# Kernel optimization log

Measured on AMD Instinct MI355X. Metric: run time of the kernel, lower is better.

The kernel has to match this reference:

```python
import jax, jax.numpy as jnp
import numpy as np

# Mamba2 hyperparams derived from init_kwargs
D_MODEL = 512
FF = 2048
D_STATE = 128
D_CONV = 4
EXPAND = 2
D_INNER = EXPAND * D_MODEL          # 1024
HEADDIM = 64                        # mamba_ssm Mamba2 default
NHEADS = D_INNER // HEADDIM         # 16
NGROUPS = 1                         # default
CONV_DIM = D_INNER + 2 * NGROUPS * D_STATE      # 1280
D_IN_PROJ = 2 * D_INNER + 2 * NGROUPS * D_STATE + NHEADS  # 2320
B_SZ = 2
SEQ = 2048


def setup_inputs() -> dict:
    key = jax.random.key(0)
    ks = jax.random.split(key, 10)
    s = 0.02
    return dict(
        tgt=jax.random.normal(ks[0], (B_SZ, SEQ, D_MODEL), jnp.float32),
        W_in=jax.random.normal(ks[1], (D_MODEL, D_IN_PROJ), jnp.float32) * s,
        conv_w=jax.random.normal(ks[2], (CONV_DIM, D_CONV), jnp.float32) * s,
        conv_b=jnp.zeros((CONV_DIM,), jnp.float32),
        dt_bias=jax.random.uniform(ks[3], (NHEADS,), jnp.float32, -4.0, -1.0),
        A_log=jnp.log(jax.random.uniform(ks[4], (NHEADS,), jnp.float32, 1.0, 16.0)),
        D_skip=jnp.ones((NHEADS,), jnp.float32),
        gnorm_w=jnp.ones((D_INNER,), jnp.float32),
        W_out=jax.random.normal(ks[5], (D_INNER, D_MODEL), jnp.float32) * s,
        n1_g=jnp.ones((D_MODEL,), jnp.float32), n1_b=jnp.zeros((D_MODEL,), jnp.float32),
        ffn_w1=jax.random.normal(ks[6], (D_MODEL, FF), jnp.float32) * s,
        ffn_b1=jnp.zeros((FF,), jnp.float32),
        ffn_w2=jax.random.normal(ks[7], (FF, D_MODEL), jnp.float32) * s,
        ffn_b2=jnp.zeros((D_MODEL,), jnp.float32),
        n3_g=jnp.ones((D_MODEL,), jnp.float32), n3_b=jnp.zeros((D_MODEL,), jnp.float32),
    )


def _layernorm(x, g, b, eps=1e-5):
    m = jnp.mean(x, -1, keepdims=True)
    v = jnp.var(x, -1, keepdims=True)
    return (x - m) * jax.lax.rsqrt(v + eps) * g + b


def _mamba2(x, W_in, conv_w, conv_b, dt_bias, A_log, D_skip, gnorm_w, W_out):
    Bb, S, _ = x.shape
    zxbcdt = x @ W_in                               # (B,S,2320)
    z = zxbcdt[..., :D_INNER]                       # gate (B,S,1024)
    xBC = zxbcdt[..., D_INNER:D_INNER + CONV_DIM]   # (B,S,1280)
    dt = zxbcdt[..., D_INNER + CONV_DIM:]           # (B,S,H)
    # causal depthwise conv1d (kernel D_CONV) + SiLU
    xc = jnp.moveaxis(xBC, 1, 2)                    # (B,C,S)
    xp = jnp.pad(xc, ((0, 0), (0, 0), (D_CONV - 1, 0)))
    yc = sum(conv_w[None, :, k:k + 1] * xp[:, :, k:k + S] for k in range(D_CONV))
    xBC = jax.nn.silu(jnp.moveaxis(yc, 1, 2) + conv_b)
    xs = xBC[..., :D_INNER].reshape(Bb, S, NHEADS, HEADDIM)   # (B,S,H,P)
    Bc = xBC[..., D_INNER:D_INNER + D_STATE]                  # (B,S,N)
    Cc = xBC[..., D_INNER + D_STATE:]                         # (B,S,N)
    dt = jax.nn.softplus(dt + dt_bias)                        # (B,S,H)
    A = -jnp.exp(A_log)                                       # (H,)
    dA = jnp.exp(dt * A)                                      # (B,S,H)
    tm = lambda a: jnp.moveaxis(a, 1, 0)                      # time-major

    def step(h, inp):
        # h: (B,H,P,N) selective state
        dA_t, dt_t, B_t, C_t, x_t = inp
        h = h * dA_t[:, :, None, None] \
            + (dt_t[:, :, None] * x_t)[..., None] * B_t[:, None, None, :]
        y_t = jnp.einsum('bhpn,bn->bhp', h, C_t)
        return h, y_t

    h0 = jnp.zeros((Bb, NHEADS, HEADDIM, D_STATE), x.dtype)
    _, ys = jax.lax.scan(step, h0, (tm(dA), tm(dt), tm(Bc), tm(Cc), tm(xs)))
    y = jnp.moveaxis(ys, 0, 1) + D_skip[None, None, :, None] * xs
    y = y.reshape(Bb, S, D_INNER)
    # gated RMSNorm (norm_before_gate=False): norm(y * silu(z)) * w
    y = y * jax.nn.silu(z)
    y = y * jax.lax.rsqrt(jnp.mean(y * y, -1, keepdims=True) + 1e-5) * gnorm_w
    return y @ W_out


def reference(tgt, W_in, conv_w, conv_b, dt_bias, A_log, D_skip, gnorm_w, W_out,
              n1_g, n1_b, ffn_w1, ffn_b1, ffn_w2, ffn_b2, n3_g, n3_b):
    t = tgt + _mamba2(tgt, W_in, conv_w, conv_b, dt_bias, A_log, D_skip, gnorm_w, W_out)
    t = _layernorm(t, n1_g, n1_b)
    h = jax.nn.gelu(t @ ffn_w1 + ffn_b1, approximate=False) @ ffn_w2 + ffn_b2
    return _layernorm(t + h, n3_g, n3_b)
```

## Files before the change

kernel.cpp:

```cpp
#include <hip/hip_runtime.h>
#include <hip/hip_bf16.h>
#include <cstddef>
#include <cstdint>

#define D_MODEL   512
#define FF        2048
#define D_STATE   128
#define D_INNER   1024
#define HEADDIM   64
#define NHEADS    16
#define CONV_DIM  1280
#define D_IN_PROJ 2320
#define NPJ_PAD   2432
#define B_SZ      2
#define SEQ       2048
#define NTOK      (B_SZ*SEQ)
#define LCH       32
#define NCHUNK    (SEQ/LCH)
#define NCID      (B_SZ*NHEADS*NCHUNK)

typedef __attribute__((ext_vector_type(8))) short short8;
typedef __attribute__((ext_vector_type(4))) float f32x4;

__device__ __forceinline__ float sigmoid_f(float x){ return 1.0f/(1.0f+expf(-x)); }
__device__ __forceinline__ float gelu_f(float x){ return 0.5f*x*(1.0f+erff(x*0.70710678118654752f)); }

__device__ __forceinline__ unsigned short bf16bits(float f){
  __hip_bfloat16 h = __float2bfloat16(f);
  return *reinterpret_cast<unsigned short*>(&h);
}
__device__ __forceinline__ float bf2f(unsigned short u){ return __uint_as_float(((unsigned)u)<<16); }
__device__ __forceinline__ float blo(unsigned u){ return __uint_as_float(u<<16); }
__device__ __forceinline__ float bhi(unsigned u){ return __uint_as_float(u & 0xffff0000u); }
__device__ __forceinline__ unsigned bfpack2(float a, float b){
  return (unsigned)bf16bits(a) | ((unsigned)bf16bits(b)<<16);
}

__device__ __forceinline__ void gload16(const void* g, void* l){
  __builtin_amdgcn_global_load_lds((const __attribute__((address_space(1))) void*)g,
                                   (__attribute__((address_space(3))) void*)l, 16, 0, 0);
}

union U4S8 { uint4 v; unsigned short s[8]; };

template<int EPI, typename OT>
__global__ __launch_bounds__(256)
void gemm128(const __hip_bfloat16* __restrict__ A, const __hip_bfloat16* __restrict__ Bt,
             const float* __restrict__ bias, OT* __restrict__ C,
             int N, int K, int ldc)
{
  __shared__ char AsRaw[128*128];
  __shared__ char BsRaw[128*128];

  const int t    = threadIdx.x;
  const int bm   = blockIdx.y * 128;
  const int bn   = blockIdx.x * 128;
  const int lane = t & 63;
  const int wid  = t >> 6;
  const int wr   = wid >> 1;
  const int wc   = wid & 1;
  const int lrow = lane & 15;
  const int lkb  = (lane >> 4) * 16;
  const int sw   = (lrow & 7) << 4;

  const int rA  = t >> 3;
  const int cbA = (t & 7) * 16;
  const int scb = cbA ^ ((rA & 7) << 4);
  const size_t strideA = (size_t)K * 2;
  const char* aSrc = (const char*)A  + (size_t)(bm + rA) * strideA + scb;
  const char* bSrc = (const char*)Bt + (size_t)(bn + rA) * strideA + scb;
  char* aDst = AsRaw + wid * 1024;
  char* bDst = BsRaw + wid * 1024;

  f32x4 acc[4][4];
  #pragma unroll
  for (int m=0;m<4;m++)
    #pragma unroll
    for (int n=0;n<4;n++) acc[m][n] = (f32x4){0.f,0.f,0.f,0.f};

  const char* ArP = AsRaw + (wr*64 + lrow) * 128;
  const char* BrP = BsRaw + (wc*64 + lrow) * 128;

  for (int k0 = 0; k0 < K; k0 += 64) {
    const size_t ko = (size_t)k0 * 2;
    gload16(aSrc + ko,               aDst);
    gload16(aSrc + ko + 32*strideA,  aDst + 4096);
    gload16(aSrc + ko + 64*strideA,  aDst + 8192);
    gload16(aSrc + ko + 96*strideA,  aDst + 12288);
    gload16(bSrc + ko,               bDst);
    gload16(bSrc + ko + 32*strideA,  bDst + 4096);
    gload16(bSrc + ko + 64*strideA,  bDst + 8192);
    gload16(bSrc + ko + 96*strideA,  bDst + 12288);
    __syncthreads();
    #pragma unroll
    for (int kk = 0; kk < 2; ++kk) {
      const int kb = (kk*64 + lkb) ^ sw;
      short8 a0 = *(const short8*)(ArP + 0*2048 + kb);
      short8 a1 = *(const short8*)(ArP + 1*2048 + kb);
      short8 a2 = *(const short8*)(ArP + 2*2048 + kb);
      short8 a3 = *(const short8*)(ArP + 3*2048 + kb);
      short8 b0 = *(const short8*)(BrP + 0*2048 + kb);
      short8 b1 = *(const short8*)(BrP + 1*2048 + kb);
      short8 b2 = *(const short8*)(BrP + 2*2048 + kb);
      short8 b3 = *(const short8*)(BrP + 3*2048 + kb);
      #pragma unroll
      for (int m=0;m<4;m++){
        short8 am = (m==0)?a0:(m==1)?a1:(m==2)?a2:a3;
        acc[m][0] = __builtin_amdgcn_mfma_f32_16x16x32_bf16(am, b0, acc[m][0], 0,0,0);
        acc[m][1] = __builtin_amdgcn_mfma_f32_16x16x32_bf16(am, b1, acc[m][1], 0,0,0);
        acc[m][2] = __builtin_amdgcn_mfma_f32_16x16x32_bf16(am, b2, acc[m][2], 0,0,0);
        acc[m][3] = __builtin_amdgcn_mfma_f32_16x16x32_bf16(am, b3, acc[m][3], 0,0,0);
      }
    }
    __syncthreads();
  }

  const int orow0 = bm + wr*64 + (lane >> 4) * 4;
  const int ocol0 = bn + wc*64 + lrow;
  #pragma unroll
  for (int n=0;n<4;n++) {
    const int col = ocol0 + n*16;
    if (col >= N) continue;
    const float bv = (EPI>=1) ? bias[col] : 0.f;
    #pragma unroll
    for (int m=0;m<4;m++) {
      #pragma unroll
      for (int j=0;j<4;j++) {
        float v = acc[m][n][j] + bv;
        if (EPI==2) v = gelu_f(v);
        OT* cp = C + (size_t)(orow0 + m*16 + j)*ldc + col;
        if constexpr (sizeof(OT)==2) *cp = __float2bfloat16(v); else *cp = v;
      }
    }
  }
}

template<int EPI, typename OT>
__global__ __launch_bounds__(256)
void gemm_bf16(const __hip_bfloat16* __restrict__ A, const __hip_bfloat16* __restrict__ Bt,
               const float* __restrict__ bias, OT* __restrict__ C,
               int N, int K, int ldc)
{
  __shared__ char AsRaw[128*128];
  __shared__ char BsRaw[64*128];

  const int t    = threadIdx.x;
  const int bm   = blockIdx.y * 128;
  const int bn   = blockIdx.x * 64;
  const int lane = t & 63;
  const int wid  = t >> 6;
  const int wr   = wid >> 1;
  const int wc   = wid & 1;
  const int lrow = lane & 15;
  const int lkb  = (lane >> 4) * 16;
  const int sw   = (lrow & 7) << 4;

  const int rA  = t >> 3;
  const int cbA = (t & 7) * 16;
  const int scb = cbA ^ ((rA & 7) << 4);
  const size_t strideA = (size_t)K * 2;
  const char* aSrc = (const char*)A  + (size_t)(bm + rA) * strideA + scb;
  const char* bSrc = (const char*)Bt + (size_t)(bn + rA) * strideA + scb;
  char* aDst = AsRaw + wid * 1024;
  char* bDst = BsRaw + wid * 1024;

  f32x4 acc[4][2];
  #pragma unroll
  for (int m=0;m<4;m++)
    #pragma unroll
    for (int n=0;n<2;n++) acc[m][n] = (f32x4){0.f,0.f,0.f,0.f};

  const char* ArP = AsRaw + (wr*64 + lrow) * 128;
  const char* BrP = BsRaw + (wc*32 + lrow) * 128;

  for (int k0 = 0; k0 < K; k0 += 64) {
    const size_t ko = (size_t)k0 * 2;
    gload16(aSrc + ko,               aDst);
    gload16(aSrc + ko + 32*strideA,  aDst + 4096);
    gload16(aSrc + ko + 64*strideA,  aDst + 8192);
    gload16(aSrc + ko + 96*strideA,  aDst + 12288);
    gload16(bSrc + ko,               bDst);
    gload16(bSrc + ko + 32*strideA,  bDst + 4096);
    __syncthreads();
    #pragma unroll
    for (int kk = 0; kk < 2; ++kk) {
      const int kb = (kk*64 + lkb) ^ sw;
      short8 a0 = *(const short8*)(ArP + 0*2048 + kb);
      short8 a1 = *(const short8*)(ArP + 1*2048 + kb);
      short8 a2 = *(const short8*)(ArP + 2*2048 + kb);
      short8 a3 = *(const short8*)(ArP + 3*2048 + kb);
      short8 b0 = *(const short8*)(BrP + 0*2048 + kb);
      short8 b1 = *(const short8*)(BrP + 1*2048 + kb);
      acc[0][0] = __builtin_amdgcn_mfma_f32_16x16x32_bf16(a0, b0, acc[0][0], 0,0,0);
      acc[1][0] = __builtin_amdgcn_mfma_f32_16x16x32_bf16(a1, b0, acc[1][0], 0,0,0);
      acc[2][0] = __builtin_amdgcn_mfma_f32_16x16x32_bf16(a2, b0, acc[2][0], 0,0,0);
      acc[3][0] = __builtin_amdgcn_mfma_f32_16x16x32_bf16(a3, b0, acc[3][0], 0,0,0);
      acc[0][1] = __builtin_amdgcn_mfma_f32_16x16x32_bf16(a0, b1, acc[0][1], 0,0,0);
      acc[1][1] = __builtin_amdgcn_mfma_f32_16x16x32_bf16(a1, b1, acc[1][1], 0,0,0);
      acc[2][1] = __builtin_amdgcn_mfma_f32_16x16x32_bf16(a2, b1, acc[2][1], 0,0,0);
      acc[3][1] = __builtin_amdgcn_mfma_f32_16x16x32_bf16(a3, b1, acc[3][1], 0,0,0);
    }
    __syncthreads();
  }

  const int orow0 = bm + wr*64 + (lane >> 4) * 4;
  const int ocol0 = bn + wc*32 + lrow;
  #pragma unroll
  for (int n=0;n<2;n++) {
    const int col = ocol0 + n*16;
    if (col >= N) continue;
    const float bv = (EPI>=1) ? bias[col] : 0.f;
    #pragma unroll
    for (int m=0;m<4;m++) {
      #pragma unroll
      for (int j=0;j<4;j++) {
        float v = acc[m][n][j] + bv;
        if (EPI==2) v = gelu_f(v);
        OT* cp = C + (size_t)(orow0 + m*16 + j)*ldc + col;
        if constexpr (sizeof(OT)==2) *cp = __float2bfloat16(v); else *cp = v;
      }
    }
  }
}

__global__ __launch_bounds__(256)
void transpose_to_bf16(const float* __restrict__ in, __hip_bfloat16* __restrict__ out,
                       int K, int N, int Npad)
{
  __shared__ float tbuf[32][33];
  const int bx = blockIdx.x * 32;
  const int by = blockIdx.y * 32;
  const int tx = threadIdx.x & 31, ty = threadIdx.x >> 5;
  #pragma unroll
  for (int u=0;u<4;u++){
    int k = by + ty + u*8;
    int n = bx + tx;
    tbuf[ty+u*8][tx] = (n < N) ? in[(size_t)k*N + n] : 0.f;
  }
  __syncthreads();
  #pragma unroll
  for (int u=0;u<4;u++){
    int n = bx + ty + u*8;
    int k = by + tx;
    if (n < Npad) out[(size_t)n*K + k] = __float2bfloat16(tbuf[tx][ty+u*8]);
  }
}

__global__ __launch_bounds__(256)
void f32_to_bf16_k(const float* __restrict__ in, __hip_bfloat16* __restrict__ out, int n)
{
  int i = (blockIdx.x*256 + threadIdx.x)*4;
  if (i < n) {
    float4 v = *(const float4*)(in + i);
    out[i+0]=__float2bfloat16(v.x); out[i+1]=__float2bfloat16(v.y);
    out[i+2]=__float2bfloat16(v.z); out[i+3]=__float2bfloat16(v.w);
  }
}

__global__ __launch_bounds__(256)
void conv_silu(const float* __restrict__ zx, const float* __restrict__ cw,
               const float* __restrict__ cb, __hip_bfloat16* __restrict__ xbc,
               const float* __restrict__ dt_bias, float* __restrict__ dtp)
{
  const int c  = blockIdx.x*256 + threadIdx.x;
  const int t0 = blockIdx.y*64;
  const int b  = blockIdx.z;
  const float w0=cw[c*4+0], w1=cw[c*4+1], w2=cw[c*4+2], w3=cw[c*4+3];
  const float cbv = cb[c];
  const float* base = zx + ((size_t)(b*SEQ + t0))*D_IN_PROJ + D_INNER + c;
  __hip_bfloat16* obase = xbc + ((size_t)(b*SEQ + t0))*CONV_DIM + c;
  float xm3, xm2, xm1;
  if (t0 == 0) { xm3 = 0.f; xm2 = 0.f; xm1 = 0.f; }
  else {
    xm3 = base[-3*(ptrdiff_t)D_IN_PROJ];
    xm2 = base[-2*(ptrdiff_t)D_IN_PROJ];
    xm1 = base[-1*(ptrdiff_t)D_IN_PROJ];
  }
  #pragma unroll 4
  for (int t=0; t<64; ++t) {
    float xc = base[(size_t)t*D_IN_PROJ];
    float acc = cbv + w0*xm3 + w1*xm2 + w2*xm1 + w3*xc;
    obase[(size_t)t*CONV_DIM] = __float2bfloat16(acc * sigmoid_f(acc));
    xm3 = xm2; xm2 = xm1; xm1 = xc;
  }
  if (blockIdx.x == 0) {
    #pragma unroll
    for (int it=0; it<4; ++it) {
      int idx = it*256 + threadIdx.x;
      int tloc = idx >> 4, hh = idx & 15;
      int tok = b*SEQ + t0 + tloc;
      float x = zx[(size_t)tok*D_IN_PROJ + (D_INNER + CONV_DIM) + hh] + dt_bias[hh];
      float sp = (x > 20.f) ? x : log1pf(expf(x));
      dtp[tok*16 + hh] = sp;
    }
  }
}

__global__ __launch_bounds__(256)
void chunk_intra(const __hip_bfloat16* __restrict__ xbc, const float* __restrict__ dtp,
                 const float* __restrict__ A_log, const float* __restrict__ D_skip,
                 float* __restrict__ y, __hip_bfloat16* __restrict__ Sbuf,
                 float* __restrict__ lcend, float* __restrict__ scl)
{
  __shared__ char sm[38912];
  __shared__ float s_dt[LCH], s_lc[LCH], s_wend[LCH];
  char* Cb  = sm;
  char* Bb  = sm + 8704;
  char* Btb = sm + 17408;
  char* Xtb = sm + 29696;
  char* Mb  = sm + 35840;

  const int cid = blockIdx.x;
  const int c  = cid & (NCHUNK-1);
  const int bh = cid >> 6;
  const int h  = bh & 15;
  const int b  = bh >> 4;
  const int tid = threadIdx.x;
  const int t0 = c*LCH;
  const __hip_bfloat16* rowbase = xbc + ((size_t)(b*SEQ + t0))*CONV_DIM;

  if (tid < 32) {
    float A_h = -expf(A_log[h]);
    float dtv = dtp[((size_t)(b*SEQ + t0 + tid))*16 + h];
    float lc = dtv * A_h;
    #pragma unroll
    for (int d=1; d<32; d<<=1) {
      float o = __shfl_up(lc, d, 32);
      if (tid >= d) lc += o;
    }
    float lc31 = __shfl(lc, 31, 32);
    s_dt[tid] = dtv;
    s_lc[tid] = lc;
    s_wend[tid] = expf(lc31 - lc) * dtv;
    scl[cid*LCH + tid] = expf(lc);
    if (tid == 31) lcend[cid] = lc;
  }

  #pragma unroll
  for (int u=0; u<2; ++u) {
    int q = tid + 256*u;
    int r = q >> 4, c8 = (q & 15)*8;
    const __hip_bfloat16* rp = rowbase + (size_t)r*CONV_DIM + D_INNER;
    *(uint4*)(Bb + r*272 + c8*2) = *(const uint4*)(rp + c8);
    *(uint4*)(Cb + r*272 + c8*2) = *(const uint4*)(rp + D_STATE + c8);
  }
  {
    int j = tid >> 3, p0 = (tid & 7)*8;
    U4S8 xv; xv.v = *(const uint4*)(rowbase + (size_t)j*CONV_DIM + h*HEADDIM + p0);
    #pragma unroll
    for (int k=0;k<8;k++)
      *(unsigned short*)(Xtb + ((p0+k)*48 + j)*2) = xv.s[k];
  }
  __syncthreads();

  #pragma unroll
  for (int u=0; u<2; ++u) {
    int q = tid + 256*u;
    int j = q >> 4, n8 = (q & 15)*8;
    const float w = s_wend[j];
    U4S8 bv; bv.v = *(const uint4*)(rowbase + (size_t)j*CONV_DIM + D_INNER + n8);
    #pragma unroll
    for (int k=0;k<8;k++)
      *(unsigned short*)(Btb + ((n8+k)*48 + j)*2) = bf16bits(bf2f(bv.s[k]) * w);
  }

  const int lane = tid & 63;
  const int w    = tid >> 6;
  const int lrow = lane & 15;
  const int lkb  = (lane >> 4) * 16;
  {
    const int wi = w >> 1, wj = w & 1;
    f32x4 g = (f32x4){0.f,0.f,0.f,0.f};
    const char* Ar = Cb + (wi*16 + lrow)*272 + lkb;
    const char* Br = Bb + (wj*16 + lrow)*272 + lkb;
    #pragma unroll
    for (int ks=0; ks<4; ks++){
      short8 a  = *(const short8*)(Ar + ks*64);
      short8 bb = *(const short8*)(Br + ks*64);
      g = __builtin_amdgcn_mfma_f32_16x16x32_bf16(a, bb, g, 0,0,0);
    }
    const int j = wj*16 + lrow;
    const float lcj = s_lc[j], dtj = s_dt[j];
    const float dsk = D_skip[h];
    const int i0 = wi*16 + (lane>>4)*4;
    #pragma unroll
    for (int r=0;r<4;r++){
      int i = i0 + r;
      float m = 0.f;
      if (j <= i) { m = g[r]*expf(s_lc[i]-lcj)*dtj; if (j==i) m += dsk; }
      *(unsigned short*)(Mb + (i*48 + j)*2) = bf16bits(m);
    }
  }
  __syncthreads();

  {
    const int it = w >> 1;
    const int pb = (w & 1)*2;
    short8 am = *(const short8*)(Mb + (it*16+lrow)*96 + lkb);
    float* ybase = y + ((size_t)(b*SEQ+t0))*D_INNER + h*HEADDIM;
    #pragma unroll
    for (int pi=0; pi<2; pi++){
      short8 xv = *(const short8*)(Xtb + ((pb+pi)*16+lrow)*96 + lkb);
      f32x4 ya = __builtin_amdgcn_mfma_f32_16x16x32_bf16(am, xv, (f32x4){0.f,0.f,0.f,0.f}, 0,0,0);
      #pragma unroll
      for (int r=0;r<4;r++){
        int i = it*16 + (lane>>4)*4 + r;
        ybase[(size_t)i*D_INNER + (pb+pi)*16 + lrow] = ya[r];
      }
    }
  }

  f32x4 sacc[8];
  {
    short8 ax = *(const short8*)(Xtb + (w*16+lrow)*96 + lkb);
    #pragma unroll
    for (int nt=0;nt<8;nt++){
      short8 bv = *(const short8*)(Btb + (nt*16+lrow)*96 + lkb);
      sacc[nt] = __builtin_amdgcn_mfma_f32_16x16x32_bf16(ax, bv, (f32x4){0.f,0.f,0.f,0.f}, 0,0,0);
    }
  }
  __syncthreads();
  {
    const int p0b = w*16 + (lane>>4)*4;
    #pragma unroll
    for (int nt=0;nt<8;nt++){
      int n = nt*16 + lrow;
      #pragma unroll
      for (int r=0;r<4;r++)
        *(unsigned short*)(sm + (p0b+r)*272 + n*2) = bf16bits(sacc[nt][r]);
    }
  }
  __syncthreads();
  __hip_bfloat16* Sout = Sbuf + (size_t)cid*(D_STATE*HEADDIM);
  #pragma unroll
  for (int u=0;u<4;u++){
    int q = tid*4+u, row = q>>4, c8 = (q&15)*8;
    *(uint4*)(Sout + row*128 + c8) = *(const uint4*)(sm + row*272 + c8*2);
  }
}

__global__ __launch_bounds__(256)
void state_scan(__hip_bfloat16* __restrict__ Sbuf, const float* __restrict__ lcend)
{
  const int bh = blockIdx.x >> 2;
  const int sl = blockIdx.x & 3;
  const int tid = threadIdx.x;
  uint4* Sb4 = (uint4*)Sbuf;
  const int idx0 = bh*NCHUNK*1024 + sl*256 + tid;

  float H[8];
  #pragma unroll
  for (int r=0;r<8;r++) H[r]=0.f;
  uint4 cur = Sb4[idx0];
  float lcv = lcend[bh*NCHUNK];
  for (int c=0;c<NCHUNK;c++){
    uint4 nxt; float lcn;
    if (c < NCHUNK-1) { nxt = Sb4[idx0 + (c+1)*1024]; lcn = lcend[bh*NCHUNK + c + 1]; }
    else              { nxt = make_uint4(0,0,0,0);    lcn = 0.f; }
    float e = expf(lcv);
    uint4 o;
    o.x = bfpack2(H[0],H[1]); o.y = bfpack2(H[2],H[3]);
    o.z = bfpack2(H[4],H[5]); o.w = bfpack2(H[6],H[7]);
    Sb4[idx0 + c*1024] = o;
    H[0]=e*H[0]+blo(cur.x); H[1]=e*H[1]+bhi(cur.x);
    H[2]=e*H[2]+blo(cur.y); H[3]=e*H[3]+bhi(cur.y);
    H[4]=e*H[4]+blo(cur.z); H[5]=e*H[5]+bhi(cur.z);
    H[6]=e*H[6]+blo(cur.w); H[7]=e*H[7]+bhi(cur.w);
    cur = nxt; lcv = lcn;
  }
}

__global__ __launch_bounds__(256)
void chunk_inter(const __hip_bfloat16* __restrict__ xbc, const __hip_bfloat16* __restrict__ Sbuf,
                 const float* __restrict__ scl, float* __restrict__ y)
{
  __shared__ char sm2[8704 + 17408];
  __shared__ float s_scl[LCH];
  char* Cb = sm2;
  char* Ht = sm2 + 8704;
  const int cid = blockIdx.x;
  const int c  = cid & (NCHUNK-1);
  const int bh = cid >> 6;
  const int h  = bh & 15;
  const int b  = bh >> 4;
  const int tid = threadIdx.x;
  const int t0 = c*LCH;
  const __hip_bfloat16* rowbase = xbc + ((size_t)(b*SEQ + t0))*CONV_DIM;

  #pragma unroll
  for (int u=0;u<2;u++){
    int q = tid + 256*u;
    int r = q >> 4, c8 = (q & 15)*8;
    *(uint4*)(Cb + r*272 + c8*2) = *(const uint4*)(rowbase + (size_t)r*CONV_DIM + D_INNER + D_STATE + c8);
  }
  const uint4* Hin = (const uint4*)(Sbuf + (size_t)cid*(D_STATE*HEADDIM));
  #pragma unroll
  for (int u=0;u<4;u++){
    int q = tid*4+u, row = q>>4, c8 = (q&15)*8;
    *(uint4*)(Ht + row*272 + c8*2) = Hin[q];
  }
  if (tid < 32) s_scl[tid] = scl[cid*LCH + tid];
  __syncthreads();

  const int lane = tid & 63;
  const int w    = tid >> 6;
  const int lrow = lane & 15;
  const int lkb  = (lane >> 4) * 16;
  const int it   = w >> 1;
  const int pb   = (w & 1)*2;
  f32x4 acc[2];
  acc[0] = (f32x4){0.f,0.f,0.f,0.f};
  acc[1] = (f32x4){0.f,0.f,0.f,0.f};
  const char* Ar = Cb + (it*16+lrow)*272 + lkb;
  const char* H0 = Ht + ((pb+0)*16+lrow)*272 + lkb;
  const char* H1 = Ht + ((pb+1)*16+lrow)*272 + lkb;
  #pragma unroll
  for (int ks=0; ks<4; ks++){
    short8 a  = *(const short8*)(Ar + ks*64);
    short8 h0 = *(const short8*)(H0 + ks*64);
    short8 h1 = *(const short8*)(H1 + ks*64);
    acc[0] = __builtin_amdgcn_mfma_f32_16x16x32_bf16(a, h0, acc[0], 0,0,0);
    acc[1] = __builtin_amdgcn_mfma_f32_16x16x32_bf16(a, h1, acc[1], 0,0,0);
  }
  float* ybase = y + ((size_t)(b*SEQ+t0))*D_INNER + h*HEADDIM;
  #pragma unroll
  for (int pi=0; pi<2; pi++){
    #pragma unroll
    for (int r=0;r<4;r++){
      int i = it*16 + (lane>>4)*4 + r;
      float* yp = ybase + (size_t)i*D_INNER + (pb+pi)*16 + lrow;
      *yp += s_scl[i]*acc[pi][r];
    }
  }
}

__global__ __launch_bounds__(256)
void gate_rms(const float* __restrict__ zx, const float* __restrict__ gw,
              const float* __restrict__ yin, __hip_bfloat16* __restrict__ ybf)
{
  int tok = blockIdx.x;
  const float* z = zx + (size_t)tok*D_IN_PROJ;
  const float* yr = yin + (size_t)tok*D_INNER;
  __hip_bfloat16* yo = ybf + (size_t)tok*D_INNER;
  float g[4];
  float ss = 0.f;
  #pragma unroll
  for (int i=0;i<4;i++) {
    int c = i*256 + threadIdx.x;
    float zv = z[c];
    float gv = yr[c] * (zv * sigmoid_f(zv));
    g[i]=gv; ss += gv*gv;
  }
  #pragma unroll
  for (int m=32;m>=1;m>>=1) ss += __shfl_xor(ss, m, 64);
  __shared__ float red[4];
  int wv = threadIdx.x >> 6;
  if ((threadIdx.x & 63)==0) red[wv]=ss;
  __syncthreads();
  float tot = red[0]+red[1]+red[2]+red[3];
  float sc = rsqrtf(tot*(1.f/1024.f) + 1e-5f);
  #pragma unroll
  for (int i=0;i<4;i++) {
    int c = i*256 + threadIdx.x;
    yo[c] = __float2bfloat16(g[i]*sc*gw[c]);
  }
}

template<int WBF>
__global__ __launch_bounds__(256)
void add_ln(const float* __restrict__ a, const float* __restrict__ bres,
            const float* __restrict__ gg, const float* __restrict__ bb,
            float* __restrict__ out, __hip_bfloat16* __restrict__ outbf)
{
  int tok = blockIdx.x;
  size_t o = (size_t)tok*D_MODEL;
  int c0 = threadIdx.x, c1 = threadIdx.x + 256;
  float v0 = a[o+c0] + bres[o+c0];
  float v1 = a[o+c1] + bres[o+c1];
  float s = v0+v1, sq = v0*v0+v1*v1;
  #pragma unroll
  for (int m=32;m>=1;m>>=1){ s += __shfl_xor(s,m,64); sq += __shfl_xor(sq,m,64); }
  __shared__ float rs[4], rq[4];
  int wv = threadIdx.x>>6;
  if ((threadIdx.x&63)==0){ rs[wv]=s; rq[wv]=sq; }
  __syncthreads();
  float S = rs[0]+rs[1]+rs[2]+rs[3];
  float Q = rq[0]+rq[1]+rq[2]+rq[3];
  float mean = S*(1.f/512.f);
  float var  = Q*(1.f/512.f) - mean*mean;
  float inv  = rsqrtf(var + 1e-5f);
  float o0 = (v0-mean)*inv*gg[c0] + bb[c0];
  float o1 = (v1-mean)*inv*gg[c1] + bb[c1];
  out[o+c0] = o0;
  out[o+c1] = o1;
  if (WBF) { outbf[o+c0] = __float2bfloat16(o0); outbf[o+c1] = __float2bfloat16(o1); }
}

extern "C" void kernel_launch(void* const* d_in, const int* in_sizes, int n_in,
                              void* d_out, int out_size, void* d_ws, size_t ws_size,
                              hipStream_t stream)
{
  const float* tgt    = (const float*)d_in[0];
  const float* W_in   = (const float*)d_in[1];
  const float* conv_w = (const float*)d_in[2];
  const float* conv_b = (const float*)d_in[3];
  const float* dt_bias= (const float*)d_in[4];
  const float* A_log  = (const float*)d_in[5];
  const float* D_skip = (const float*)d_in[6];
  const float* gnorm_w= (const float*)d_in[7];
  const float* W_out  = (const float*)d_in[8];
  const float* n1_g   = (const float*)d_in[9];
  const float* n1_b   = (const float*)d_in[10];
  const float* ffn_w1 = (const float*)d_in[11];
  const float* ffn_b1 = (const float*)d_in[12];
  const float* ffn_w2 = (const float*)d_in[13];
  const float* ffn_b2 = (const float*)d_in[14];
  const float* n3_g   = (const float*)d_in[15];
  const float* n3_b   = (const float*)d_in[16];
  float* out = (float*)d_out;
  float* ws  = (float*)d_ws;

  float* zx   = ws;
  float* xbcF = zx  + (size_t)NTOK*D_IN_PROJ;
  __hip_bfloat16* xbc = (__hip_bfloat16*)xbcF;
  float* dtp  = xbcF + 2621440;
  float* yb   = dtp + (size_t)NTOK*16;
  float* Sreg = yb  + (size_t)NTOK*D_INNER;
  __hip_bfloat16* Sbuf = (__hip_bfloat16*)Sreg;
  float* lcend= Sreg + 8388608;
  float* scl  = lcend + NCID;

  __hip_bfloat16* tgt_bf = (__hip_bfloat16*)yb;
  __hip_bfloat16* Wint   = (__hip_bfloat16*)Sreg;
  __hip_bfloat16* yb_bf  = (__hip_bfloat16*)xbcF;
  __hip_bfloat16* tb_bf  = (__hip_bfloat16*)(yb + 2097152);
  float* tb   = Sreg;
  float* tmp  = Sreg + 2097152;
  __hip_bfloat16* Woutt  = (__hip_bfloat16*)(Sreg + 4194304);
  __hip_bfloat16* W1t    = (__hip_bfloat16*)(Sreg + 4194304 + 262144);
  __hip_bfloat16* W2t    = (__hip_bfloat16*)(Sreg + 4194304 + 262144 + 524288);
  __hip_bfloat16* hmid_bf= (__hip_bfloat16*)zx;

  transpose_to_bf16<<<dim3(NPJ_PAD/32, D_MODEL/32), 256, 0, stream>>>(W_in, Wint, D_MODEL, D_IN_PROJ, NPJ_PAD);
  f32_to_bf16_k<<<(NTOK*D_MODEL)/1024, 256, 0, stream>>>(tgt, tgt_bf, NTOK*D_MODEL);
  gemm128<0,float><<<dim3(NPJ_PAD/128, NTOK/128), 256, 0, stream>>>(
      tgt_bf, Wint, nullptr, zx, D_IN_PROJ, D_MODEL, D_IN_PROJ);
  conv_silu<<<dim3(CONV_DIM/256, SEQ/64, B_SZ), 256, 0, stream>>>(zx, conv_w, conv_b, xbc, dt_bias, dtp);
  chunk_intra<<<NCID, 256, 0, stream>>>(xbc, dtp, A_log, D_skip, yb, Sbuf, lcend, scl);
  state_scan<<<B_SZ*NHEADS*4, 256, 0, stream>>>(Sbuf, lcend);
  chunk_inter<<<NCID, 256, 0, stream>>>(xbc, Sbuf, scl, yb);
  transpose_to_bf16<<<dim3(D_MODEL/32, D_INNER/32), 256, 0, stream>>>(W_out, Woutt, D_INNER, D_MODEL, D_MODEL);
  transpose_to_bf16<<<dim3(FF/32, D_MODEL/32), 256, 0, stream>>>(ffn_w1, W1t, D_MODEL, FF, FF);
  transpose_to_bf16<<<dim3(D_MODEL/32, FF/32), 256, 0, stream>>>(ffn_w2, W2t, FF, D_MODEL, D_MODEL);
  gate_rms<<<NTOK, 256, 0, stream>>>(zx, gnorm_w, yb, yb_bf);
  gemm_bf16<0,float><<<dim3(D_MODEL/64, NTOK/128), 256, 0, stream>>>(
      yb_bf, Woutt, nullptr, tmp, D_MODEL, D_INNER, D_MODEL);
  add_ln<1><<<NTOK, 256, 0, stream>>>(tmp, tgt, n1_g, n1_b, tb, tb_bf);
  gemm128<2,__hip_bfloat16><<<dim3(FF/128, NTOK/128), 256, 0, stream>>>(
      tb_bf, W1t, ffn_b1, hmid_bf, FF, D_MODEL, FF);
  gemm_bf16<1,float><<<dim3(D_MODEL/64, NTOK/128), 256, 0, stream>>>(
      hmid_bf, W2t, ffn_b2, tmp, D_MODEL, FF, D_MODEL);
  add_ln<0><<<NTOK, 256, 0, stream>>>(tmp, tb, n3_g, n3_b, out, nullptr);
}
```

Measured before the change: 212.0 us.

## Split-K the narrow GEMMs, merge prep kernels, vectorize gate_rms, deepen scan prefetch

```diff
diff --git a/kernel.cpp b/kernel.cpp
--- a/kernel.cpp
+++ b/kernel.cpp
@@ -139,7 +139,7 @@
 __global__ __launch_bounds__(256)
 void gemm_bf16(const __hip_bfloat16* __restrict__ A, const __hip_bfloat16* __restrict__ Bt,
                const float* __restrict__ bias, OT* __restrict__ C,
-               int N, int K, int ldc)
+               int N, int K, int ldc, int M, int nsplit)
 {
   __shared__ char AsRaw[128*128];
   __shared__ char BsRaw[64*128];
@@ -147,6 +147,12 @@
   const int t    = threadIdx.x;
   const int bm   = blockIdx.y * 128;
   const int bn   = blockIdx.x * 64;
+  const int z    = blockIdx.z;
+  const int Kloop= K / nsplit;
+  A += (size_t)z * Kloop;
+  Bt += (size_t)z * Kloop;
+  C += (size_t)z * M * ldc;
+
   const int lane = t & 63;
   const int wid  = t >> 6;
   const int wr   = wid >> 1;
@@ -173,7 +179,7 @@
   const char* ArP = AsRaw + (wr*64 + lrow) * 128;
   const char* BrP = BsRaw + (wc*32 + lrow) * 128;
 
-  for (int k0 = 0; k0 < K; k0 += 64) {
+  for (int k0 = 0; k0 < Kloop; k0 += 64) {
     const size_t ko = (size_t)k0 * 2;
     gload16(aSrc + ko,               aDst);
     gload16(aSrc + ko + 32*strideA,  aDst + 4096);
@@ -209,7 +215,7 @@
   for (int n=0;n<2;n++) {
     const int col = ocol0 + n*16;
     if (col >= N) continue;
-    const float bv = (EPI>=1) ? bias[col] : 0.f;
+    const float bv = (EPI>=1 && z==0) ? bias[col] : 0.f;
     #pragma unroll
     for (int m=0;m<4;m++) {
       #pragma unroll
@@ -223,38 +229,49 @@
   }
 }
 
-__global__ __launch_bounds__(256)
-void transpose_to_bf16(const float* __restrict__ in, __hip_bfloat16* __restrict__ out,
-                       int K, int N, int Npad)
+__device__ __forceinline__ void tr_tile(const float* __restrict__ in,
+                                        __hip_bfloat16* __restrict__ out,
+                                        int K, int N, int Npad, int bx, int by)
 {
   __shared__ float tbuf[32][33];
-  const int bx = blockIdx.x * 32;
-  const int by = blockIdx.y * 32;
   const int tx = threadIdx.x & 31, ty = threadIdx.x >> 5;
   #pragma unroll
   for (int u=0;u<4;u++){
-    int k = by + ty + u*8;
-    int n = bx + tx;
+    int k = by*32 + ty + u*8;
+    int n = bx*32 + tx;
     tbuf[ty+u*8][tx] = (n < N) ? in[(size_t)k*N + n] : 0.f;
   }
   __syncthreads();
   #pragma unroll
   for (int u=0;u<4;u++){
-    int n = bx + ty + u*8;
-    int k = by + tx;
+    int n = bx*32 + ty + u*8;
+    int k = by*32 + tx;
     if (n < Npad) out[(size_t)n*K + k] = __float2bfloat16(tbuf[tx][ty+u*8]);
   }
 }
 
 __global__ __launch_bounds__(256)
-void f32_to_bf16_k(const float* __restrict__ in, __hip_bfloat16* __restrict__ out, int n)
-{
-  int i = (blockIdx.x*256 + threadIdx.x)*4;
-  if (i < n) {
-    float4 v = *(const float4*)(in + i);
-    out[i+0]=__float2bfloat16(v.x); out[i+1]=__float2bfloat16(v.y);
-    out[i+2]=__float2bfloat16(v.z); out[i+3]=__float2bfloat16(v.w);
-  }
+void prep_all(const float* __restrict__ tgt, __hip_bfloat16* __restrict__ tgt_bf,
+              const float* __restrict__ W_in,  __hip_bfloat16* __restrict__ Wint,
+              const float* __restrict__ W_out, __hip_bfloat16* __restrict__ Woutt,
+              const float* __restrict__ W1,    __hip_bfloat16* __restrict__ W1t,
+              const float* __restrict__ W2,    __hip_bfloat16* __restrict__ W2t)
+{
+  int bid = blockIdx.x;
+  if (bid < 2048) {
+    int i = bid*1024 + threadIdx.x*4;
+    float4 v = *(const float4*)(tgt + i);
+    *(uint2*)(tgt_bf + i) = (uint2){bfpack2(v.x,v.y), bfpack2(v.z,v.w)};
+    return;
+  }
+  bid -= 2048;
+  if (bid < 76*16) { tr_tile(W_in, Wint, D_MODEL, D_IN_PROJ, NPJ_PAD, bid%76, bid/76); return; }
+  bid -= 76*16;
+  if (bid < 16*32) { tr_tile(W_out, Woutt, D_INNER, D_MODEL, D_MODEL, bid%16, bid/16); return; }
+  bid -= 16*32;
+  if (bid < 64*16) { tr_tile(W1, W1t, D_MODEL, FF, FF, bid%64, bid/64); return; }
+  bid -= 64*16;
+  tr_tile(W2, W2t, FF, D_MODEL, D_MODEL, bid%16, bid/16);
 }
 
 __global__ __launch_bounds__(256)
@@ -452,12 +469,14 @@
   #pragma unroll
   for (int r=0;r<8;r++) H[r]=0.f;
   uint4 cur = Sb4[idx0];
-  float lcv = lcend[bh*NCHUNK];
+  uint4 nx1 = Sb4[idx0 + 1024];
+  float lc0 = lcend[bh*NCHUNK];
+  float lc1 = lcend[bh*NCHUNK + 1];
   for (int c=0;c<NCHUNK;c++){
-    uint4 nxt; float lcn;
-    if (c < NCHUNK-1) { nxt = Sb4[idx0 + (c+1)*1024]; lcn = lcend[bh*NCHUNK + c + 1]; }
-    else              { nxt = make_uint4(0,0,0,0);    lcn = 0.f; }
-    float e = expf(lcv);
+    uint4 nx2; float lc2;
+    if (c + 2 < NCHUNK) { nx2 = Sb4[idx0 + (c+2)*1024]; lc2 = lcend[bh*NCHUNK + c + 2]; }
+    else                { nx2 = make_uint4(0,0,0,0);    lc2 = 0.f; }
+    float e = expf(lc0);
     uint4 o;
     o.x = bfpack2(H[0],H[1]); o.y = bfpack2(H[2],H[3]);
     o.z = bfpack2(H[4],H[5]); o.w = bfpack2(H[6],H[7]);
@@ -466,7 +485,7 @@
     H[2]=e*H[2]+blo(cur.y); H[3]=e*H[3]+bhi(cur.y);
     H[4]=e*H[4]+blo(cur.z); H[5]=e*H[5]+bhi(cur.z);
     H[6]=e*H[6]+blo(cur.w); H[7]=e*H[7]+bhi(cur.w);
-    cur = nxt; lcv = lcn;
+    cur = nx1; nx1 = nx2; lc0 = lc1; lc1 = lc2;
   }
 }
 
@@ -539,18 +558,14 @@
               const float* __restrict__ yin, __hip_bfloat16* __restrict__ ybf)
 {
   int tok = blockIdx.x;
-  const float* z = zx + (size_t)tok*D_IN_PROJ;
-  const float* yr = yin + (size_t)tok*D_INNER;
-  __hip_bfloat16* yo = ybf + (size_t)tok*D_INNER;
-  float g[4];
-  float ss = 0.f;
-  #pragma unroll
-  for (int i=0;i<4;i++) {
-    int c = i*256 + threadIdx.x;
-    float zv = z[c];
-    float gv = yr[c] * (zv * sigmoid_f(zv));
-    g[i]=gv; ss += gv*gv;
-  }
+  int c = threadIdx.x*4;
+  float4 zv = *(const float4*)(zx + (size_t)tok*D_IN_PROJ + c);
+  float4 yv = *(const float4*)(yin + (size_t)tok*D_INNER + c);
+  float g0 = yv.x * (zv.x * sigmoid_f(zv.x));
+  float g1 = yv.y * (zv.y * sigmoid_f(zv.y));
+  float g2 = yv.z * (zv.z * sigmoid_f(zv.z));
+  float g3 = yv.w * (zv.w * sigmoid_f(zv.w));
+  float ss = g0*g0 + g1*g1 + g2*g2 + g3*g3;
   #pragma unroll
   for (int m=32;m>=1;m>>=1) ss += __shfl_xor(ss, m, 64);
   __shared__ float red[4];
@@ -559,24 +574,23 @@
   __syncthreads();
   float tot = red[0]+red[1]+red[2]+red[3];
   float sc = rsqrtf(tot*(1.f/1024.f) + 1e-5f);
-  #pragma unroll
-  for (int i=0;i<4;i++) {
-    int c = i*256 + threadIdx.x;
-    yo[c] = __float2bfloat16(g[i]*sc*gw[c]);
-  }
+  float4 gwv = *(const float4*)(gw + c);
+  *(uint2*)(ybf + (size_t)tok*D_INNER + c) =
+      (uint2){bfpack2(g0*sc*gwv.x, g1*sc*gwv.y), bfpack2(g2*sc*gwv.z, g3*sc*gwv.w)};
 }
 
 template<int WBF>
 __global__ __launch_bounds__(256)
-void add_ln(const float* __restrict__ a, const float* __restrict__ bres,
+void add_ln(const float* __restrict__ a0p, const float* __restrict__ a1p,
+            const float* __restrict__ bres,
             const float* __restrict__ gg, const float* __restrict__ bb,
             float* __restrict__ out, __hip_bfloat16* __restrict__ outbf)
 {
   int tok = blockIdx.x;
   size_t o = (size_t)tok*D_MODEL;
   int c0 = threadIdx.x, c1 = threadIdx.x + 256;
-  float v0 = a[o+c0] + bres[o+c0];
-  float v1 = a[o+c1] + bres[o+c1];
+  float v0 = a0p[o+c0] + a1p[o+c0] + bres[o+c0];
+  float v1 = a0p[o+c1] + a1p[o+c1] + bres[o+c1];
   float s = v0+v1, sq = v0*v0+v1*v1;
   #pragma unroll
   for (int m=32;m>=1;m>>=1){ s += __shfl_xor(s,m,64); sq += __shfl_xor(sq,m,64); }
@@ -624,41 +638,40 @@
   float* xbcF = zx  + (size_t)NTOK*D_IN_PROJ;
   __hip_bfloat16* xbc = (__hip_bfloat16*)xbcF;
   float* dtp  = xbcF + 2621440;
-  float* yb   = dtp + (size_t)NTOK*16;
-  float* Sreg = yb  + (size_t)NTOK*D_INNER;
+  float* yb   = dtp + 65536;
+  float* Sreg = yb  + 4194304;
   __hip_bfloat16* Sbuf = (__hip_bfloat16*)Sreg;
   float* lcend= Sreg + 8388608;
   float* scl  = lcend + NCID;
-
-  __hip_bfloat16* tgt_bf = (__hip_bfloat16*)yb;
-  __hip_bfloat16* Wint   = (__hip_bfloat16*)Sreg;
-  __hip_bfloat16* yb_bf  = (__hip_bfloat16*)xbcF;
-  __hip_bfloat16* tb_bf  = (__hip_bfloat16*)(yb + 2097152);
+  float* wreg = scl + 65536;
+  __hip_bfloat16* Wint  = (__hip_bfloat16*)wreg;
+  __hip_bfloat16* Woutt = (__hip_bfloat16*)(wreg + 622592);
+  __hip_bfloat16* W1t   = (__hip_bfloat16*)(wreg + 622592+262144);
+  __hip_bfloat16* W2t   = (__hip_bfloat16*)(wreg + 622592+262144+524288);
+  __hip_bfloat16* tgt_bf= (__hip_bfloat16*)(wreg + 622592+262144+524288+524288);
+
+  __hip_bfloat16* yb_bf = (__hip_bfloat16*)xbcF;
+  __hip_bfloat16* tb_bf = (__hip_bfloat16*)yb;
   float* tb   = Sreg;
-  float* tmp  = Sreg + 2097152;
-  __hip_bfloat16* Woutt  = (__hip_bfloat16*)(Sreg + 4194304);
-  __hip_bfloat16* W1t    = (__hip_bfloat16*)(Sreg + 4194304 + 262144);
-  __hip_bfloat16* W2t    = (__hip_bfloat16*)(Sreg + 4194304 + 262144 + 524288);
-  __hip_bfloat16* hmid_bf= (__hip_bfloat16*)zx;
-
-  transpose_to_bf16<<<dim3(NPJ_PAD/32, D_MODEL/32), 256, 0, stream>>>(W_in, Wint, D_MODEL, D_IN_PROJ, NPJ_PAD);
-  f32_to_bf16_k<<<(NTOK*D_MODEL)/1024, 256, 0, stream>>>(tgt, tgt_bf, NTOK*D_MODEL);
+  float* tmp0 = Sreg + 2097152;
+  float* tmp1 = Sreg + 4194304;
+  __hip_bfloat16* hmid_bf = (__hip_bfloat16*)zx;
+
+  prep_all<<<2048 + 76*16 + 16*32 + 64*16 + 16*64, 256, 0, stream>>>(
+      tgt, tgt_bf, W_in, Wint, W_out, Woutt, ffn_w1, W1t, ffn_w2, W2t);
   gemm128<0,float><<<dim3(NPJ_PAD/128, NTOK/128), 256, 0, stream>>>(
       tgt_bf, Wint, nullptr, zx, D_IN_PROJ, D_MODEL, D_IN_PROJ);
   conv_silu<<<dim3(CONV_DIM/256, SEQ/64, B_SZ), 256, 0, stream>>>(zx, conv_w, conv_b, xbc, dt_bias, dtp);
   chunk_intra<<<NCID, 256, 0, stream>>>(xbc, dtp, A_log, D_skip, yb, Sbuf, lcend, scl);
   state_scan<<<B_SZ*NHEADS*4, 256, 0, stream>>>(Sbuf, lcend);
   chunk_inter<<<NCID, 256, 0, stream>>>(xbc, Sbuf, scl, yb);
-  transpose_to_bf16<<<dim3(D_MODEL/32, D_INNER/32), 256, 0, stream>>>(W_out, Woutt, D_INNER, D_MODEL, D_MODEL);
-  transpose_to_bf16<<<dim3(FF/32, D_MODEL/32), 256, 0, stream>>>(ffn_w1, W1t, D_MODEL, FF, FF);
-  transpose_to_bf16<<<dim3(D_MODEL/32, FF/32), 256, 0, stream>>>(ffn_w2, W2t, FF, D_MODEL, D_MODEL);
   gate_rms<<<NTOK, 256, 0, stream>>>(zx, gnorm_w, yb, yb_bf);
-  gemm_bf16<0,float><<<dim3(D_MODEL/64, NTOK/128), 256, 0, stream>>>(
-      yb_bf, Woutt, nullptr, tmp, D_MODEL, D_INNER, D_MODEL);
-  add_ln<1><<<NTOK, 256, 0, stream>>>(tmp, tgt, n1_g, n1_b, tb, tb_bf);
+  gemm_bf16<0,float><<<dim3(D_MODEL/64, NTOK/128, 2), 256, 0, stream>>>(
+      yb_bf, Woutt, nullptr, tmp0, D_MODEL, D_INNER, D_MODEL, NTOK, 2);
+  add_ln<1><<<NTOK, 256, 0, stream>>>(tmp0, tmp1, tgt, n1_g, n1_b, tb, tb_bf);
   gemm128<2,__hip_bfloat16><<<dim3(FF/128, NTOK/128), 256, 0, stream>>>(
       tb_bf, W1t, ffn_b1, hmid_bf, FF, D_MODEL, FF);
-  gemm_bf16<1,float><<<dim3(D_MODEL/64, NTOK/128), 256, 0, stream>>>(
-      hmid_bf, W2t, ffn_b2, tmp, D_MODEL, FF, D_MODEL);
-  add_ln<0><<<NTOK, 256, 0, stream>>>(tmp, tb, n3_g, n3_b, out, nullptr);
-}
+  gemm_bf16<1,float><<<dim3(D_MODEL/64, NTOK/128, 2), 256, 0, stream>>>(
+      hmid_bf, W2t, ffn_b2, tmp0, D_MODEL, FF, D_MODEL, NTOK, 2);
+  add_ln<0><<<NTOK, 256, 0, stream>>>(tmp0, tmp1, tb, n3_g, n3_b, out, nullptr);
+}
```

After: 181.2 us. 1.17x faster.
